# Kernel optimization log

Hardware: AMD Instinct MI355X
Metric: run time of the kernel (lower is better)

The kernel has to match this reference:

```python
import jax, jax.numpy as jnp
import numpy as np

N, F = 4096, 256  # nodes, in_features == hidden_features == out_features; num_heads = 1
LN_EPS = 1e-5
L1_EPS = 1e-12


def setup_inputs() -> dict:
    key = jax.random.key(0)
    k0, k1, k2, k3, k4 = jax.random.split(key, 5)
    h = jax.random.normal(k0, (N, F), jnp.float32)
    x = jax.random.normal(k1, (N, F), jnp.float32)
    s = 1.0 / np.sqrt(F)
    s_v = 1.0 / np.sqrt(F + 3)
    # torch Linear weight layout: [out_features, in_features]
    w_k = jax.random.uniform(k2, (F, F), jnp.float32, -s, s)
    w_q = jax.random.uniform(k3, (F, F), jnp.float32, -s, s)
    w_v = jax.random.uniform(k4, (F, F + 3), jnp.float32, -s_v, s_v)
    # mixing init: ones * semantic_weight(-1.0), row 0 zeroed
    mixing = jnp.full((2, 2), -1.0, jnp.float32).at[0].set(0.0)
    ln_gamma = jnp.ones((F,), jnp.float32)
    ln_beta = jnp.zeros((F,), jnp.float32)
    return {"h": h, "x": x, "w_k": w_k, "w_q": w_q, "w_v": w_v,
            "mixing": mixing, "ln_gamma": ln_gamma, "ln_beta": ln_beta}


def reference(h, x, w_k, w_q, w_v, mixing, ln_gamma, ln_beta):
    h0, x0 = h, x
    # LayerNorm (biased variance, eps=1e-5)
    mu = h.mean(-1, keepdims=True)
    var = ((h - mu) ** 2).mean(-1, keepdims=True)
    hn = (h - mu) * jax.lax.rsqrt(var + LN_EPS) * ln_gamma + ln_beta
    # F.normalize(x, p=1): divide by max(L1 norm, eps)
    xn = x / jnp.maximum(jnp.abs(x).sum(-1, keepdims=True), L1_EPS)
    # projections (single head: [N, F])
    k = hn @ w_k.T
    q = hn @ w_q.T
    # feature-attention: softmax over last dim of k q^T / sqrt(F)
    a_h = jax.nn.softmax((k @ q.T) * (F ** -0.5), axis=-1)          # [N, N]
    # x-affinity
    a_x = xn @ xn.T                                                  # [N, N]
    # stats of a_x rows: diag, sum, std (unbiased, ddof=1)
    i = jnp.stack([jnp.diagonal(a_x), a_x.sum(-1), a_x.std(-1, ddof=1)], axis=-1)  # [N, 3]
    # learned 2x2 mixing, softmax over dim 0 (columns)
    m = jax.nn.softmax(mixing, axis=0)
    a_x2 = a_x * m[0, 0] + a_h * m[1, 0]
    a_h2 = a_x * m[0, 1] + a_h * m[1, 1]
    # torch a_h.transpose(-1, 0) swaps the row axis with the head axis,
    # transposing the NxN matrix (head dim = 1): h <- a_h2^T @ hn
    h_agg = a_h2.T @ hn                                              # [N, F]
    x_out = a_x2 @ xn                                                # [N, F]
    h_out = jax.nn.elu(jnp.concatenate([h_agg, i], axis=-1) @ w_v.T)
    return (h_out + h0, x_out + x0)
```

## Files before the change

kernel.cpp:

```cpp
#include <hip/hip_runtime.h>
#include <cstdint>
#include <cstddef>

#define NB 4096
#define FD 256

typedef __attribute__((ext_vector_type(4))) float f32x4;
typedef __attribute__((ext_vector_type(8))) short bf16x8;

__device__ __forceinline__ ushort f2bf(float f) {
  union { float f; uint32_t u; } v; v.f = f;
  uint32_t r = v.u + 0x7fffu + ((v.u >> 16) & 1u);
  return (ushort)(r >> 16);
}
__device__ __forceinline__ float bf2f(ushort b) {
  union { uint32_t u; float f; } v; v.u = ((uint32_t)b) << 16;
  return v.f;
}

__device__ __forceinline__ void gld16(const void* g, void* l) {
  __builtin_amdgcn_global_load_lds(
      (const __attribute__((address_space(1))) char*)g,
      (__attribute__((address_space(3))) char*)l, 16, 0, 0);
}

__device__ __forceinline__ float wave_reduce_sum(float v) {
#pragma unroll
  for (int off = 32; off >= 1; off >>= 1) v += __shfl_xor(v, off);
  return v;
}
__device__ __forceinline__ float wave_reduce_max(float v) {
#pragma unroll
  for (int off = 32; off >= 1; off >>= 1) v = fmaxf(v, __shfl_xor(v, off));
  return v;
}

__global__ __launch_bounds__(256) void rownorm_wcast_kernel(
    const float* __restrict__ h, const float* __restrict__ x,
    const float* __restrict__ gamma, const float* __restrict__ beta,
    ushort* __restrict__ hnb, ushort* __restrict__ xnb, float* __restrict__ diag,
    const float* __restrict__ w_k, const float* __restrict__ w_q,
    const float* __restrict__ w_v,
    ushort* __restrict__ wkqb, ushort* __restrict__ wvAb,
    float* __restrict__ wvbT3) {
  __shared__ float rA[4], rB[4], rC[4], rD[4];
  if (blockIdx.x >= NB) {
    const int r = blockIdx.x - NB, t = threadIdx.x;
    wkqb[r * 256 + t] = f2bf(w_k[r * 256 + t]);
    wkqb[(256 + r) * 256 + t] = f2bf(w_q[r * 256 + t]);
    wvAb[r * 256 + t] = f2bf(w_v[(size_t)r * 259 + t]);
    if (t < 3) wvbT3[t * 256 + r] = w_v[(size_t)r * 259 + 256 + t];
    return;
  }
  const int r = blockIdx.x, t = threadIdx.x, wid = t >> 6, lane = t & 63;
  const size_t base = (size_t)r * FD + t;
  const float hv = h[base], xv = x[base];
  float s1 = wave_reduce_sum(hv);
  float s2 = wave_reduce_sum(hv * hv);
  float a1 = wave_reduce_sum(fabsf(xv));
  float q1 = wave_reduce_sum(xv * xv);
  if (lane == 0) { rA[wid] = s1; rB[wid] = s2; rC[wid] = a1; rD[wid] = q1; }
  __syncthreads();
  const float S1 = rA[0] + rA[1] + rA[2] + rA[3];
  const float S2 = rB[0] + rB[1] + rB[2] + rB[3];
  const float L1 = rC[0] + rC[1] + rC[2] + rC[3];
  const float Q1 = rD[0] + rD[1] + rD[2] + rD[3];
  const float mu = S1 * (1.0f / FD);
  const float var = S2 * (1.0f / FD) - mu * mu;
  const float rstd = rsqrtf(var + 1e-5f);
  const float d = fmaxf(L1, 1e-12f), dinv = 1.0f / d;
  hnb[base] = f2bf((hv - mu) * rstd * gamma[t] + beta[t]);
  xnb[base] = f2bf(xv * dinv);
  if (t == 0) diag[r] = Q1 * dinv * dinv;
}

__global__ __launch_bounds__(256) void transpose2_kernel(
    const ushort* __restrict__ inA, ushort* __restrict__ outA,
    const ushort* __restrict__ inB, ushort* __restrict__ outB, int R, int C) {
  __shared__ ushort tile[64][65];
  const ushort* in = blockIdx.z ? inB : inA;
  ushort* out = blockIdx.z ? outB : outA;
  const int bc = blockIdx.x * 64, br = blockIdx.y * 64;
  const int t = threadIdx.x;
#pragma unroll
  for (int i = 0; i < 16; ++i) {
    const int idx = t + 256 * i;
    const int rr = idx >> 6, cc = idx & 63;
    tile[rr][cc] = in[(size_t)(br + rr) * C + bc + cc];
  }
  __syncthreads();
#pragma unroll
  for (int i = 0; i < 16; ++i) {
    const int idx = t + 256 * i;
    const int rr = idx >> 6, cc = idx & 63;
    out[(size_t)(bc + rr) * R + br + cc] = tile[cc][rr];
  }
}

__global__ __launch_bounds__(256) void transpose4_kernel(
    const ushort* __restrict__ in, ushort* __restrict__ out, int R, int C) {
  __shared__ ushort tile[64][66];
  const int bc = blockIdx.x * 64, br = blockIdx.y * 64;
  const int t = threadIdx.x;
  const int c4 = (t & 15) * 4;
  const int r0 = t >> 4;
#pragma unroll
  for (int i = 0; i < 4; ++i) {
    const int rr = r0 + 16 * i;
    *(ushort4*)&tile[rr][c4] =
        *(const ushort4*)(in + (size_t)(br + rr) * C + bc + c4);
  }
  __syncthreads();
#pragma unroll
  for (int i = 0; i < 4; ++i) {
    const int ro = r0 + 16 * i;
    ushort4 o;
    o.x = tile[c4 + 0][ro];
    o.y = tile[c4 + 1][ro];
    o.z = tile[c4 + 2][ro];
    o.w = tile[c4 + 3][ro];
    *(ushort4*)(out + (size_t)(bc + ro) * R + br + c4) = o;
  }
}

__global__ __launch_bounds__(256) void colsum_kernel(
    const ushort* __restrict__ xnT, float* __restrict__ s) {
  __shared__ float red[4];
  const int f = blockIdx.x, t = threadIdx.x, wid = t >> 6, lane = t & 63;
  float a = 0.f;
#pragma unroll
  for (int i = 0; i < 16; ++i) a += bf2f(xnT[(size_t)f * NB + t + 256 * i]);
  a = wave_reduce_sum(a);
  if (lane == 0) red[wid] = a;
  __syncthreads();
  if (t == 0) s[f] = red[0] + red[1] + red[2] + red[3];
}

__global__ __launch_bounds__(256) void reduce16g_kernel(
    const float* __restrict__ in, ushort* __restrict__ t23B,
    ushort* __restrict__ M2T) {
  const int idx = blockIdx.x * 256 + threadIdx.x;
  const int i = idx >> 9, j = idx & 511;
  float a = 0.f;
#pragma unroll
  for (int z = 0; z < 16; ++z) a += in[(size_t)z * (256 * 512) + idx];
  if (j < 256) t23B[i * 256 + j] = f2bf(a);
  else M2T[i * 256 + (j - 256)] = f2bf(a);
}

__global__ __launch_bounds__(256) void softmax_kernel(
    const ushort* __restrict__ S, ushort* __restrict__ P) {
  __shared__ float red[4];
  const int r = blockIdx.x, t = threadIdx.x, wid = t >> 6, lane = t & 63;
  const uint4* Sr = (const uint4*)(S + (size_t)r * NB);
  float v[16];
  float lmax = -1e30f;
#pragma unroll
  for (int i = 0; i < 2; ++i) {
    const uint4 c = Sr[t + 256 * i];
    const uint32_t w4[4] = {c.x, c.y, c.z, c.w};
#pragma unroll
    for (int j = 0; j < 4; ++j) {
      v[i * 8 + j * 2]     = bf2f((ushort)(w4[j] & 0xffffu));
      v[i * 8 + j * 2 + 1] = bf2f((ushort)(w4[j] >> 16));
    }
  }
#pragma unroll
  for (int u = 0; u < 16; ++u) lmax = fmaxf(lmax, v[u]);
  lmax = wave_reduce_max(lmax);
  if (lane == 0) red[wid] = lmax;
  __syncthreads();
  const float gmax = fmaxf(fmaxf(red[0], red[1]), fmaxf(red[2], red[3]));
  __syncthreads();
  float lsum = 0.f;
#pragma unroll
  for (int u = 0; u < 16; ++u) { v[u] = __expf(v[u] - gmax); lsum += v[u]; }
  lsum = wave_reduce_sum(lsum);
  if (lane == 0) red[wid] = lsum;
  __syncthreads();
  const float pinv = 1.f / (red[0] + red[1] + red[2] + red[3]);
  uint4* Pr = (uint4*)(P + (size_t)r * NB);
#pragma unroll
  for (int i = 0; i < 2; ++i) {
    uint4 o;
    o.x = (uint32_t)f2bf(v[i*8+0] * pinv) | ((uint32_t)f2bf(v[i*8+1] * pinv) << 16);
    o.y = (uint32_t)f2bf(v[i*8+2] * pinv) | ((uint32_t)f2bf(v[i*8+3] * pinv) << 16);
    o.z = (uint32_t)f2bf(v[i*8+4] * pinv) | ((uint32_t)f2bf(v[i*8+5] * pinv) << 16);
    o.w = (uint32_t)f2bf(v[i*8+6] * pinv) | ((uint32_t)f2bf(v[i*8+7] * pinv) << 16);
    Pr[t + 256 * i] = o;
  }
}

__global__ __launch_bounds__(256) void megacombine_kernel(
    const ushort* __restrict__ px, const ushort* __restrict__ ph,
    const float* __restrict__ t23, const ushort* __restrict__ xnb,
    const float* __restrict__ sv, const float* __restrict__ diag,
    const float* __restrict__ x, const float* __restrict__ h,
    const float* __restrict__ wvbT3, const float* __restrict__ mix,
    float* __restrict__ out_x, float* __restrict__ out_h) {
  __shared__ float rA[4], rB[4];
  const size_t NF = (size_t)NB * FD;
  const int i = blockIdx.x, f = threadIdx.x, wid = f >> 6, lane = f & 63;
  const float e0x = __expf(mix[0]), e1x = __expf(mix[2]);
  const float mAx = e0x / (e0x + e1x), mBx = e1x / (e0x + e1x);
  const float e0h = __expf(mix[1]), e1h = __expf(mix[3]);
  const float mAh = e0h / (e0h + e1h), mBh = e1h / (e0h + e1h);

  const size_t rowoff = (size_t)i * FD + f;
  float ax = 0.f, ah = 0.f;
#pragma unroll
  for (int z = 0; z < 4; ++z) {
    ax += bf2f(px[(size_t)z * NF + rowoff]);
    ah += bf2f(ph[(size_t)z * NF + rowoff]);
  }
  const float t2v = t23[(size_t)i * 512 + f];
  const float t3v = t23[(size_t)i * 512 + 256 + f];
  const float xv = bf2f(xnb[rowoff]);

  float rs = wave_reduce_sum(xv * sv[f]);
  float rq = wave_reduce_sum(xv * t2v);
  if (lane == 0) { rA[wid] = rs; rB[wid] = rq; }
  __syncthreads();
  rs = rA[0] + rA[1] + rA[2] + rA[3];
  rq = rB[0] + rB[1] + rB[2] + rB[3];
  const float mean = rs * (1.0f / NB);
  const float var = (rq - (float)NB * mean * mean) * (1.0f / (NB - 1));
  const float sd = sqrtf(fmaxf(var, 0.f));
  const float dg = diag[i];
  const float statsterm = dg * wvbT3[f] + rs * wvbT3[256 + f] + sd * wvbT3[512 + f];

  out_x[rowoff] = mBx * ax + mAx * t2v + x[rowoff];
  const float pre = mBh * ah + mAh * t3v + statsterm;
  out_h[rowoff] = ((pre > 0.f) ? pre : expm1f(pre)) + h[rowoff];
}

struct GDesc {
  const ushort* A; const ushort* B; void* C;
  int lda, ldb, ldc, K, gx, gy, epi;
  float alpha; long pstride; int nb;
};

__global__ __launch_bounds__(256) void gemm_batch3(
    GDesc d0, GDesc d1, GDesc d2, int ntot) {
  int flat = blockIdx.x;
  flat = (flat & 7) * (ntot >> 3) + (flat >> 3);
  GDesc d; int l;
  if (flat < d0.nb) { d = d0; l = flat; }
  else if (flat < d0.nb + d1.nb) { d = d1; l = flat - d0.nb; }
  else { d = d2; l = flat - d0.nb - d1.nb; }
  const int bx = l % d.gx;
  const int rest = l / d.gx;
  const int by = rest % d.gy, bz = rest / d.gy;

  __shared__ __align__(16) ushort At[2][64][32];
  __shared__ __align__(16) ushort Bt[2][64][32];
  const int tid = threadIdx.x;
  const int wave = tid >> 6, lane = tid & 63;
  const int wr = wave >> 1, wc = wave & 1;
  const int bi = by * 64, bj = bx * 64;
  const int fr = lane & 15, fq = lane >> 4;
  const int sub = lane >> 2, q = lane & 3;

  f32x4 acc[2][2];
#pragma unroll
  for (int m = 0; m < 2; ++m)
#pragma unroll
    for (int n = 0; n < 2; ++n) acc[m][n] = (f32x4){0.f, 0.f, 0.f, 0.f};

  const int kbase = bz * d.K;
  const int kend = kbase + d.K;

  auto stage = [&](int bufi, int k0) {
    {
      const int row = wave * 16 + sub;
      const int qs = q ^ (row & 3);
      gld16(d.A + (size_t)(bi + row) * d.lda + k0 + qs * 8, &At[bufi][wave * 16][0]);
    }
    {
      const int row = wave * 16 + sub;
      const int qs = q ^ (row & 3);
      gld16(d.B + (size_t)(bj + row) * d.ldb + k0 + qs * 8, &Bt[bufi][wave * 16][0]);
    }
  };

  stage(0, kbase);
  __syncthreads();

  int cur = 0;
  for (int k0 = kbase; k0 < kend; k0 += 32) {
    if (k0 + 32 < kend) stage(cur ^ 1, k0 + 32);
    bf16x8 a[2], b[2];
#pragma unroll
    for (int m = 0; m < 2; ++m) {
      const int row = wr * 32 + m * 16 + fr;
      a[m] = *(const bf16x8*)((const char*)&At[cur][row][0] + ((fq ^ (row & 3)) * 16));
    }
#pragma unroll
    for (int n = 0; n < 2; ++n) {
      const int row = wc * 32 + n * 16 + fr;
      b[n] = *(const bf16x8*)((const char*)&Bt[cur][row][0] + ((fq ^ (row & 3)) * 16));
    }
#pragma unroll
    for (int m = 0; m < 2; ++m)
#pragma unroll
      for (int n = 0; n < 2; ++n)
        acc[m][n] = __builtin_amdgcn_mfma_f32_16x16x32_bf16(a[m], b[n], acc[m][n], 0, 0, 0);
    __syncthreads();
    cur ^= 1;
  }

#pragma unroll
  for (int m = 0; m < 2; ++m)
#pragma unroll
    for (int n = 0; n < 2; ++n)
#pragma unroll
      for (int r = 0; r < 4; ++r) {
        const int row = bi + wr * 32 + m * 16 + fq * 4 + r;
        const int col = bj + wc * 32 + n * 16 + fr;
        const size_t ci = (size_t)row * d.ldc + col;
        const float v = acc[m][n][r];
        if (d.epi == 1) ((ushort*)d.C)[ci] = f2bf(v * d.alpha);
        else ((float*)d.C)[(size_t)bz * d.pstride + ci] = v;
      }
}

__global__ __launch_bounds__(256) void gemm_agg(
    const ushort* __restrict__ P, const ushort* __restrict__ PT,
    const ushort* __restrict__ xnT, const ushort* __restrict__ hvT,
    ushort* __restrict__ px, ushort* __restrict__ ph) {
  __shared__ __align__(16) ushort At[2][128][32];
  __shared__ __align__(16) ushort Bt[2][128][32];
  const int tid = threadIdx.x;
  const int wave = tid >> 6, lane = tid & 63;
  const int wr = wave >> 1, wc = wave & 1;

  const int nwg = 512;
  int flat = blockIdx.x + 2 * (blockIdx.y + 32 * blockIdx.z);
  flat = (flat & 7) * (nwg >> 3) + (flat >> 3);
  const int bx = flat % 2, by = (flat / 2) % 32, bz = flat / 64;
  const int sel = bz >> 2, kz = bz & 3;

  const ushort* A = sel ? PT : P;
  const ushort* B = sel ? hvT : xnT;
  ushort* C = sel ? ph : px;

  const int bi = by * 128, bj = bx * 128;
  const int fr = lane & 15, fq = lane >> 4;
  const int sub = lane >> 2, q = lane & 3;

  f32x4 acc[4][4];
#pragma unroll
  for (int m = 0; m < 4; ++m)
#pragma unroll
    for (int n = 0; n < 4; ++n) acc[m][n] = (f32x4){0.f, 0.f, 0.f, 0.f};

  const int kbase = kz * 1024;
  const int kend = kbase + 1024;

  auto stage = [&](int bufi, int k0) {
    for (int c = wave; c < 8; c += 4) {
      const int row = c * 16 + sub;
      const int qs = q ^ (row & 3);
      gld16(A + (size_t)(bi + row) * NB + k0 + qs * 8, &At[bufi][c * 16][0]);
    }
    for (int c = wave; c < 8; c += 4) {
      const int row = c * 16 + sub;
      const int qs = q ^ (row & 3);
      gld16(B + (size_t)(bj + row) * NB + k0 + qs * 8, &Bt[bufi][c * 16][0]);
    }
  };

  stage(0, kbase);
  __syncthreads();

  int cur = 0;
  for (int k0 = kbase; k0 < kend; k0 += 32) {
    if (k0 + 32 < kend) stage(cur ^ 1, k0 + 32);
    bf16x8 a[4], b[4];
#pragma unroll
    for (int m = 0; m < 4; ++m) {
      const int row = wr * 64 + m * 16 + fr;
      a[m] = *(const bf16x8*)((const char*)&At[cur][row][0] + ((fq ^ (row & 3)) * 16));
    }
#pragma unroll
    for (int n = 0; n < 4; ++n) {
      const int row = wc * 64 + n * 16 + fr;
      b[n] = *(const bf16x8*)((const char*)&Bt[cur][row][0] + ((fq ^ (row & 3)) * 16));
    }
#pragma unroll
    for (int m = 0; m < 4; ++m)
#pragma unroll
      for (int n = 0; n < 4; ++n)
        acc[m][n] = __builtin_amdgcn_mfma_f32_16x16x32_bf16(a[m], b[n], acc[m][n], 0, 0, 0);
    __syncthreads();
    cur ^= 1;
  }

#pragma unroll
  for (int m = 0; m < 4; ++m)
#pragma unroll
    for (int n = 0; n < 4; ++n)
#pragma unroll
      for (int r = 0; r < 4; ++r) {
        const int row = bi + wr * 64 + m * 16 + fq * 4 + r;
        const int col = bj + wc * 64 + n * 16 + fr;
        C[(size_t)kz * ((size_t)NB * FD) + (size_t)row * FD + col] = f2bf(acc[m][n][r]);
      }
}

template <int BM, int BN, int EPI>
__global__ __launch_bounds__(256) void gemm_nt(
    const ushort* __restrict__ A, int lda,
    const ushort* __restrict__ B, int ldb,
    void* __restrict__ Cp, int ldc, int K, float alpha,
    size_t pstride) {
  constexpr int WAVES_N = (BM <= 32) ? 4 : 2;
  constexpr int WAVES_M = 4 / WAVES_N;
  constexpr int WM = BM / WAVES_M, WN = BN / WAVES_N;
  constexpr int MR = WM / 16, NR = WN / 16;
  __shared__ __align__(16) ushort At[2][BM][32];
  __shared__ __align__(16) ushort Bt[2][BN][32];
  const int tid = threadIdx.x;
  const int wave = tid >> 6, lane = tid & 63;
  const int wr = wave / WAVES_N, wc = wave % WAVES_N;

  const int gx = gridDim.x, gy = gridDim.y;
  const int nwg = gx * gy * gridDim.z;
  int flat = blockIdx.x + gx * (blockIdx.y + gy * blockIdx.z);
  if ((nwg & 7) == 0) flat = (flat & 7) * (nwg >> 3) + (flat >> 3);
  const int bx = flat % gx, by = (flat / gx) % gy, bz = flat / (gx * gy);

  const int bi = by * BM, bj = bx * BN;
  const int fr = lane & 15, fq = lane >> 4;
  const int sub = lane >> 2, q = lane & 3;

  f32x4 acc[MR][NR];
#pragma unroll
  for (int m = 0; m < MR; ++m)
#pragma unroll
    for (int n = 0; n < NR; ++n) acc[m][n] = (f32x4){0.f, 0.f, 0.f, 0.f};

  const int kbase = (EPI >= 5) ? bz * K : 0;
  const int kend = kbase + K;

  auto stage = [&](int bufi, int k0) {
    for (int c = wave; c < BM / 16; c += 4) {
      const int row = c * 16 + sub;
      const int qs = q ^ (row & 3);
      gld16(A + (size_t)(bi + row) * lda + k0 + qs * 8, &At[bufi][c * 16][0]);
    }
    for (int c = wave; c < BN / 16; c += 4) {
      const int row = c * 16 + sub;
      const int qs = q ^ (row & 3);
      gld16(B + (size_t)(bj + row) * ldb + k0 + qs * 8, &Bt[bufi][c * 16][0]);
    }
  };

  stage(0, kbase);
  __syncthreads();

  int cur = 0;
  for (int k0 = kbase; k0 < kend; k0 += 32) {
    if (k0 + 32 < kend) stage(cur ^ 1, k0 + 32);
    bf16x8 a[MR], b[NR];
#pragma unroll
    for (int m = 0; m < MR; ++m) {
      const int row = wr * WM + m * 16 + fr;
      a[m] = *(const bf16x8*)((const char*)&At[cur][row][0] + ((fq ^ (row & 3)) * 16));
    }
#pragma unroll
    for (int n = 0; n < NR; ++n) {
      const int row = wc * WN + n * 16 + fr;
      b[n] = *(const bf16x8*)((const char*)&Bt[cur][row][0] + ((fq ^ (row & 3)) * 16));
    }
#pragma unroll
    for (int m = 0; m < MR; ++m)
#pragma unroll
      for (int n = 0; n < NR; ++n)
        acc[m][n] = __builtin_amdgcn_mfma_f32_16x16x32_bf16(a[m], b[n], acc[m][n], 0, 0, 0);
    __syncthreads();
    cur ^= 1;
  }

#pragma unroll
  for (int m = 0; m < MR; ++m)
#pragma unroll
    for (int n = 0; n < NR; ++n)
#pragma unroll
      for (int r = 0; r < 4; ++r) {
        const int row = bi + wr * WM + m * 16 + fq * 4 + r;
        const int col = bj + wc * WN + n * 16 + fr;
        const size_t ci = (size_t)row * ldc + col;
        const float v = acc[m][n][r];
        if (EPI == 0) ((float*)Cp)[ci] = v * alpha;
        else if (EPI == 1) ((ushort*)Cp)[ci] = f2bf(v * alpha);
        else if (EPI == 5) ((float*)Cp)[(size_t)bz * pstride + ci] = v;
        else if (EPI == 6) ((ushort*)Cp)[(size_t)bz * pstride + ci] = f2bf(v);
      }
}

extern "C" void kernel_launch(void* const* d_in, const int* in_sizes, int n_in,
                              void* d_out, int out_size, void* d_ws, size_t ws_size,
                              hipStream_t stream) {
  const float* h      = (const float*)d_in[0];
  const float* x      = (const float*)d_in[1];
  const float* w_k    = (const float*)d_in[2];
  const float* w_q    = (const float*)d_in[3];
  const float* w_v    = (const float*)d_in[4];
  const float* mixing = (const float*)d_in[5];
  const float* gamma  = (const float*)d_in[6];
  const float* beta   = (const float*)d_in[7];

  float* out_h = (float*)d_out;
  float* out_x = out_h + (size_t)NB * FD;

  char* w = (char*)d_ws;
  ushort* S     = (ushort*)(w + 0);
  ushort* P     = (ushort*)(w + 33554432);
  ushort* PT    = (ushort*)(w + 67108864);
  ushort* hnb   = (ushort*)(w + 100663296);
  ushort* xnb   = (ushort*)(w + 102760448);
  ushort* xnbT  = (ushort*)(w + 104857600);
  ushort* hnbT  = (ushort*)(w + 106954752);
  ushort* kq    = (ushort*)(w + 109051904);
  ushort* hvT   = (ushort*)(w + 113246208);
  float*  t23   = (float*)(w + 115343360);
  ushort* t23B  = (ushort*)(w + 123731968);
  ushort* M2T   = (ushort*)(w + 123994112);
  ushort* wkqb  = (ushort*)(w + 124125184);
  ushort* wvAb  = (ushort*)(w + 124387328);
  float*  wvbT3 = (float*)(w + 124518400);
  float*  diag  = (float*)(w + 124521472);
  float*  sv    = (float*)(w + 124537856);
  float*  Gramp = (float*)(w + 67108864);
  ushort* px    = (ushort*)(w + 0);
  ushort* ph    = (ushort*)(w + 16777216);

  rownorm_wcast_kernel<<<NB + FD, 256, 0, stream>>>(
      h, x, gamma, beta, hnb, xnb, diag, w_k, w_q, w_v, wkqb, wvAb, wvbT3);
  transpose2_kernel<<<dim3(FD / 64, NB / 64, 2), 256, 0, stream>>>(
      xnb, xnbT, hnb, hnbT, NB, FD);
  colsum_kernel<<<FD, 256, 0, stream>>>(xnbT, sv);

  {
    GDesc dkq = {hnb, wkqb, kq, FD, FD, 512, FD, 8, 64, 1, 1.f, 0, 512};
    GDesc dgr = {xnbT, xnbT, Gramp, NB, NB, 512, NB / 16, 8, 4, 5, 1.f,
                 (long)(256 * 512), 512};
    GDesc dhv = {wvAb, hnb, hvT, FD, FD, NB, FD, 64, 4, 1, 1.f, 0, 256};
    gemm_batch3<<<1280, 256, 0, stream>>>(dkq, dgr, dhv, 1280);
  }
  reduce16g_kernel<<<256 * 512 / 256, 256, 0, stream>>>(Gramp, t23B, M2T);

  gemm_nt<64, 64, 1><<<dim3(4, 4), 256, 0, stream>>>(
      wvAb, FD, M2T, FD, t23B + 256 * 256, FD, FD, 1.f, 0);

  gemm_nt<64, 64, 0><<<dim3(512 / 64, NB / 64), 256, 0, stream>>>(
      xnb, FD, t23B, FD, t23, 512, FD, 1.f, 0);

  gemm_nt<128, 128, 1><<<dim3(NB / 128, NB / 128), 256, 0, stream>>>(
      kq, 512, kq + 256, 512, S, NB, FD, 0.0625f, 0);

  softmax_kernel<<<NB, 256, 0, stream>>>(S, P);
  transpose4_kernel<<<dim3(NB / 64, NB / 64), 256, 0, stream>>>(P, PT, NB, NB);

  gemm_agg<<<dim3(2, 32, 8), 256, 0, stream>>>(P, PT, xnbT, hvT, px, ph);

  megacombine_kernel<<<NB, 256, 0, stream>>>(
      px, ph, t23, xnb, sv, diag, x, h, wvbT3, mixing, out_x, out_h);
}
```

Baseline: 123.4 us.

## Use 64-wide K tiles in big GEMMs and batch score and t23 GEMMs

Adds a shared 128x128 GEMM body that stages 64-wide K slices with an 8-way XOR swizzle, which halves the number of barrier and loop iterations per tile. gemm_agg is switched to this body. The score GEMM (kq·kqᵀ) and the t23 GEMM are merged into one batched launch with a swizzled block order, removing a launch and letting the small GEMM fill otherwise idle CUs. The generic gemm_nt is simplified by dropping its unused split-K and remap paths. The cost is double the LDS per block, which may lower occupancy.

```diff
diff --git a/kernel.cpp b/kernel.cpp
--- a/kernel.cpp
+++ b/kernel.cpp
@@ -324,12 +324,55 @@
       }
 }
 
+#define GEMM128_BODY(APTR, BPTR, LDA, LDB, KBASE, KEND)                        \
+  f32x4 acc[4][4];                                                             \
+  _Pragma("unroll") for (int m = 0; m < 4; ++m)                                \
+      _Pragma("unroll") for (int n = 0; n < 4; ++n)                            \
+          acc[m][n] = (f32x4){0.f, 0.f, 0.f, 0.f};                             \
+  auto stage = [&](int bufi, int k0) {                                         \
+    for (int c = wave; c < 16; c += 4) {                                       \
+      const int row = c * 8 + sub8;                                            \
+      const int qs = q8 ^ (row & 7);                                           \
+      gld16(APTR + (size_t)(bi + row) * LDA + k0 + qs * 8, &At[bufi][c * 8][0]); \
+    }                                                                          \
+    for (int c = wave; c < 16; c += 4) {                                       \
+      const int row = c * 8 + sub8;                                            \
+      const int qs = q8 ^ (row & 7);                                           \
+      gld16(BPTR + (size_t)(bj + row) * LDB + k0 + qs * 8, &Bt[bufi][c * 8][0]); \
+    }                                                                          \
+  };                                                                           \
+  stage(0, KBASE);                                                             \
+  __syncthreads();                                                             \
+  int cur = 0;                                                                 \
+  for (int k0 = KBASE; k0 < KEND; k0 += 64) {                                  \
+    if (k0 + 64 < KEND) stage(cur ^ 1, k0 + 64);                               \
+    _Pragma("unroll") for (int ks = 0; ks < 2; ++ks) {                         \
+      bf16x8 a[4], b[4];                                                       \
+      _Pragma("unroll") for (int m = 0; m < 4; ++m) {                          \
+        const int row = wr * 64 + m * 16 + fr;                                 \
+        const int ch = (ks * 4 + fq) ^ (row & 7);                              \
+        a[m] = *(const bf16x8*)((const char*)&At[cur][row][0] + ch * 16);      \
+      }                                                                        \
+      _Pragma("unroll") for (int n = 0; n < 4; ++n) {                          \
+        const int row = wc * 64 + n * 16 + fr;                                 \
+        const int ch = (ks * 4 + fq) ^ (row & 7);                              \
+        b[n] = *(const bf16x8*)((const char*)&Bt[cur][row][0] + ch * 16);      \
+      }                                                                        \
+      _Pragma("unroll") for (int m = 0; m < 4; ++m)                            \
+          _Pragma("unroll") for (int n = 0; n < 4; ++n)                        \
+              acc[m][n] = __builtin_amdgcn_mfma_f32_16x16x32_bf16(             \
+                  a[m], b[n], acc[m][n], 0, 0, 0);                             \
+    }                                                                          \
+    __syncthreads();                                                           \
+    cur ^= 1;                                                                  \
+  }
+
 __global__ __launch_bounds__(256) void gemm_agg(
     const ushort* __restrict__ P, const ushort* __restrict__ PT,
     const ushort* __restrict__ xnT, const ushort* __restrict__ hvT,
     ushort* __restrict__ px, ushort* __restrict__ ph) {
-  __shared__ __align__(16) ushort At[2][128][32];
-  __shared__ __align__(16) ushort Bt[2][128][32];
+  __shared__ __align__(16) ushort At[2][128][64];
+  __shared__ __align__(16) ushort Bt[2][128][64];
   const int tid = threadIdx.x;
   const int wave = tid >> 6, lane = tid & 63;
   const int wr = wave >> 1, wc = wave & 1;
@@ -346,55 +389,12 @@
 
   const int bi = by * 128, bj = bx * 128;
   const int fr = lane & 15, fq = lane >> 4;
-  const int sub = lane >> 2, q = lane & 3;
-
-  f32x4 acc[4][4];
-#pragma unroll
-  for (int m = 0; m < 4; ++m)
-#pragma unroll
-    for (int n = 0; n < 4; ++n) acc[m][n] = (f32x4){0.f, 0.f, 0.f, 0.f};
+  const int sub8 = lane >> 3, q8 = lane & 7;
 
   const int kbase = kz * 1024;
   const int kend = kbase + 1024;
 
-  auto stage = [&](int bufi, int k0) {
-    for (int c = wave; c < 8; c += 4) {
-      const int row = c * 16 + sub;
-      const int qs = q ^ (row & 3);
-      gld16(A + (size_t)(bi + row) * NB + k0 + qs * 8, &At[bufi][c * 16][0]);
-    }
-    for (int c = wave; c < 8; c += 4) {
-      const int row = c * 16 + sub;
-      const int qs = q ^ (row & 3);
-      gld16(B + (size_t)(bj + row) * NB + k0 + qs * 8, &Bt[bufi][c * 16][0]);
-    }
-  };
-
-  stage(0, kbase);
-  __syncthreads();
-
-  int cur = 0;
-  for (int k0 = kbase; k0 < kend; k0 += 32) {
-    if (k0 + 32 < kend) stage(cur ^ 1, k0 + 32);
-    bf16x8 a[4], b[4];
-#pragma unroll
-    for (int m = 0; m < 4; ++m) {
-      const int row = wr * 64 + m * 16 + fr;
-      a[m] = *(const bf16x8*)((const char*)&At[cur][row][0] + ((fq ^ (row & 3)) * 16));
-    }
-#pragma unroll
-    for (int n = 0; n < 4; ++n) {
-      const int row = wc * 64 + n * 16 + fr;
-      b[n] = *(const bf16x8*)((const char*)&Bt[cur][row][0] + ((fq ^ (row & 3)) * 16));
-    }
-#pragma unroll
-    for (int m = 0; m < 4; ++m)
-#pragma unroll
-      for (int n = 0; n < 4; ++n)
-        acc[m][n] = __builtin_amdgcn_mfma_f32_16x16x32_bf16(a[m], b[n], acc[m][n], 0, 0, 0);
-    __syncthreads();
-    cur ^= 1;
-  }
+  GEMM128_BODY(A, B, NB, NB, kbase, kend)
 
 #pragma unroll
   for (int m = 0; m < 4; ++m)
@@ -405,6 +405,47 @@
         const int row = bi + wr * 64 + m * 16 + fq * 4 + r;
         const int col = bj + wc * 64 + n * 16 + fr;
         C[(size_t)kz * ((size_t)NB * FD) + (size_t)row * FD + col] = f2bf(acc[m][n][r]);
+      }
+}
+
+struct GD2 {
+  const ushort* A; const ushort* B; void* C;
+  int lda, ldb, ldc, K, gx, epi;
+  float alpha; int nb;
+};
+
+__global__ __launch_bounds__(256) void gemm_batch2big(GD2 d0, GD2 d1, int ntot) {
+  __shared__ __align__(16) ushort At[2][128][64];
+  __shared__ __align__(16) ushort Bt[2][128][64];
+  const int tid = threadIdx.x;
+  const int wave = tid >> 6, lane = tid & 63;
+  const int wr = wave >> 1, wc = wave & 1;
+
+  int flat = blockIdx.x;
+  flat = (flat & 7) * (ntot >> 3) + (flat >> 3);
+  GD2 d; int l;
+  if (flat < d0.nb) { d = d0; l = flat; }
+  else { d = d1; l = flat - d0.nb; }
+  const int bx = l % d.gx, by = l / d.gx;
+
+  const int bi = by * 128, bj = bx * 128;
+  const int fr = lane & 15, fq = lane >> 4;
+  const int sub8 = lane >> 3, q8 = lane & 7;
+
+  GEMM128_BODY(d.A, d.B, d.lda, d.ldb, 0, d.K)
+
+#pragma unroll
+  for (int m = 0; m < 4; ++m)
+#pragma unroll
+    for (int n = 0; n < 4; ++n)
+#pragma unroll
+      for (int r = 0; r < 4; ++r) {
+        const int row = bi + wr * 64 + m * 16 + fq * 4 + r;
+        const int col = bj + wc * 64 + n * 16 + fr;
+        const size_t ci = (size_t)row * d.ldc + col;
+        const float v = acc[m][n][r];
+        if (d.epi == 1) ((ushort*)d.C)[ci] = f2bf(v * d.alpha);
+        else ((float*)d.C)[ci] = v;
       }
 }
 
@@ -414,8 +455,7 @@
     const ushort* __restrict__ B, int ldb,
     void* __restrict__ Cp, int ldc, int K, float alpha,
     size_t pstride) {
-  constexpr int WAVES_N = (BM <= 32) ? 4 : 2;
-  constexpr int WAVES_M = 4 / WAVES_N;
+  constexpr int WAVES_N = 2, WAVES_M = 2;
   constexpr int WM = BM / WAVES_M, WN = BN / WAVES_N;
   constexpr int MR = WM / 16, NR = WN / 16;
   __shared__ __align__(16) ushort At[2][BM][32];
@@ -424,12 +464,7 @@
   const int wave = tid >> 6, lane = tid & 63;
   const int wr = wave / WAVES_N, wc = wave % WAVES_N;
 
-  const int gx = gridDim.x, gy = gridDim.y;
-  const int nwg = gx * gy * gridDim.z;
-  int flat = blockIdx.x + gx * (blockIdx.y + gy * blockIdx.z);
-  if ((nwg & 7) == 0) flat = (flat & 7) * (nwg >> 3) + (flat >> 3);
-  const int bx = flat % gx, by = (flat / gx) % gy, bz = flat / (gx * gy);
-
+  const int bx = blockIdx.x, by = blockIdx.y;
   const int bi = by * BM, bj = bx * BN;
   const int fr = lane & 15, fq = lane >> 4;
   const int sub = lane >> 2, q = lane & 3;
@@ -439,9 +474,6 @@
   for (int m = 0; m < MR; ++m)
 #pragma unroll
     for (int n = 0; n < NR; ++n) acc[m][n] = (f32x4){0.f, 0.f, 0.f, 0.f};
-
-  const int kbase = (EPI >= 5) ? bz * K : 0;
-  const int kend = kbase + K;
 
   auto stage = [&](int bufi, int k0) {
     for (int c = wave; c < BM / 16; c += 4) {
@@ -456,12 +488,12 @@
     }
   };
 
-  stage(0, kbase);
+  stage(0, 0);
   __syncthreads();
 
   int cur = 0;
-  for (int k0 = kbase; k0 < kend; k0 += 32) {
-    if (k0 + 32 < kend) stage(cur ^ 1, k0 + 32);
+  for (int k0 = 0; k0 < K; k0 += 32) {
+    if (k0 + 32 < K) stage(cur ^ 1, k0 + 32);
     bf16x8 a[MR], b[NR];
 #pragma unroll
     for (int m = 0; m < MR; ++m) {
@@ -493,9 +525,7 @@
         const size_t ci = (size_t)row * ldc + col;
         const float v = acc[m][n][r];
         if (EPI == 0) ((float*)Cp)[ci] = v * alpha;
-        else if (EPI == 1) ((ushort*)Cp)[ci] = f2bf(v * alpha);
-        else if (EPI == 5) ((float*)Cp)[(size_t)bz * pstride + ci] = v;
-        else if (EPI == 6) ((ushort*)Cp)[(size_t)bz * pstride + ci] = f2bf(v);
+        else ((ushort*)Cp)[ci] = f2bf(v * alpha);
       }
 }
 
@@ -554,11 +584,11 @@
   gemm_nt<64, 64, 1><<<dim3(4, 4), 256, 0, stream>>>(
       wvAb, FD, M2T, FD, t23B + 256 * 256, FD, FD, 1.f, 0);
 
-  gemm_nt<64, 64, 0><<<dim3(512 / 64, NB / 64), 256, 0, stream>>>(
-      xnb, FD, t23B, FD, t23, 512, FD, 1.f, 0);
-
-  gemm_nt<128, 128, 1><<<dim3(NB / 128, NB / 128), 256, 0, stream>>>(
-      kq, 512, kq + 256, 512, S, NB, FD, 0.0625f, 0);
+  {
+    GD2 dS  = {kq, kq + 256, S, 512, 512, NB, FD, 32, 1, 0.0625f, 1024};
+    GD2 dT  = {xnb, t23B, t23, FD, FD, 512, FD, 4, 0, 1.f, 128};
+    gemm_batch2big<<<1152, 256, 0, stream>>>(dS, dT, 1152);
+  }
 
   softmax_kernel<<<NB, 256, 0, stream>>>(S, P);
   transpose4_kernel<<<dim3(NB / 64, NB / 64), 256, 0, stream>>>(P, PT, NB, NB);
```

Measured after the change: 117.7 us. -4.7%, faster.
